# Optimization experiments

Hardware: AMD Instinct MI355X
Metric: run time of the kernel (lower is better)

The kernel has to match this reference:

```python
import jax, jax.numpy as jnp
import numpy as np

NUM_HEADS = 12

def setup_inputs() -> dict:
    key = jax.random.key(0)
    k1, k2 = jax.random.split(key)
    X = jax.random.normal(k1, (2, 2048, 768), dtype=jnp.float32)
    # torch nn.Linear(dim, 2*dim, bias=False) weight has shape [2*dim, dim]
    W_qkv = jax.random.normal(k2, (1536, 768), dtype=jnp.float32) * (768 ** -0.5)
    return {"X": X, "W_qkv": W_qkv}

def reference(X, W_qkv):
    B, N, C = X.shape
    H = NUM_HEADS
    hd = C // H
    scale = hd ** -0.5
    # qkv: [B, N, 2, H, hd]
    qkv = (X @ W_qkv.T).reshape(B, N, 2, H, hd)
    q = jnp.transpose(qkv[:, :, 0], (0, 2, 1, 3))  # [B, H, N, hd]
    k = jnp.transpose(qkv[:, :, 1], (0, 2, 1, 3))  # [B, H, N, hd]
    attn = jnp.einsum('bhnd,bhmd->bhnm', q, k) * scale  # [B, H, N, N]
    # dropout p=0 -> identity; double sum over heads and keys
    scores = attn.sum(axis=1).sum(axis=-1)  # [B, N]
    return scores
```

## Files before the change

kernel.cpp:

```cpp
#include <hip/hip_runtime.h>


#define DIM 768
#define SEQ 2048
#define NGRP 8
#define NBLK 512
#define PBASE 0xAAAAAAAAu


__global__ __launch_bounds__(256, 2)
void fused_k(const float* __restrict__ X, const float* __restrict__ W,
             float* __restrict__ out, float* __restrict__ ws) {
    float* xpart = ws;
    float* t     = ws + 2 * NGRP * DIM;
    unsigned* cw   = (unsigned*)(ws + 16384);
    unsigned* root = cw + 512;
    unsigned* cnt2 = cw + 544;

    __shared__ alignas(16) float sbuf[DIM];
    __shared__ float vloc[24];

    const int bi   = blockIdx.x;
    const int tid  = threadIdx.x;
    const int lane = tid & 63;
    const int wv   = tid >> 6;

    {
        int b  = bi >> 8;
        int ch = bi & 255;
        int g  = ch >> 5;
        if (tid < 192) {
            const float4* base =
                (const float4*)(X + ((size_t)b * SEQ + (size_t)ch * 8) * DIM) + tid;
            float4 a = {0.f, 0.f, 0.f, 0.f};
            #pragma unroll
            for (int n = 0; n < 8; ++n) {
                float4 x = base[n * 192];
                a.x += x.x; a.y += x.y; a.z += x.z; a.w += x.w;
            }
            float* dst = xpart + (size_t)(b * NGRP + g) * DIM + tid * 4;
            atomicAdd(dst + 0, a.x);
            atomicAdd(dst + 1, a.y);
            atomicAdd(dst + 2, a.z);
            atomicAdd(dst + 3, a.w);
        }
    }
    __syncthreads();
    if (tid == 0) {
        unsigned* leaf = cw + (bi & 15) * 32;
        unsigned old = __hip_atomic_fetch_add(leaf, 1u, __ATOMIC_RELAXED,
                                              __HIP_MEMORY_SCOPE_AGENT);
        if (old == PBASE + 31)
            __hip_atomic_fetch_add(root, 1u, __ATOMIC_RELAXED,
                                   __HIP_MEMORY_SCOPE_AGENT);
    }

    if (bi < 64) {
        if (tid == 0) {
            int guard = 0;
            while (__hip_atomic_load(root, __ATOMIC_RELAXED,
                                     __HIP_MEMORY_SCOPE_AGENT) != PBASE + 16) {
                __builtin_amdgcn_s_sleep(1);
                if (++guard > (1 << 24)) break;
            }
        }
        __syncthreads();

        int b     = bi >> 5;
        int chunk = bi & 31;
        int c0    = chunk * 24;

        #pragma unroll
        for (int k = 0; k < 3; ++k) {
            int d = tid + k * 256;
            const float* p = xpart + (size_t)(b * NGRP) * DIM + d;
            float s = 0.f;
            #pragma unroll
            for (int g = 0; g < NGRP; ++g)
                s += p[(size_t)g * DIM];
            sbuf[d] = s;
        }
        __syncthreads();

        const float4* xs4 = (const float4*)sbuf;
        #pragma unroll
        for (int ic = 0; ic < 6; ++ic) {
            int c = c0 + wv * 6 + ic;
            const float4* wr = (const float4*)(W + (size_t)(DIM + c) * DIM);
            float acc = 0.f;
            #pragma unroll
            for (int j = 0; j < 3; ++j) {
                float4 a = wr[lane + 64 * j];
                float4 s = xs4[lane + 64 * j];
                acc += a.x * s.x + a.y * s.y + a.z * s.z + a.w * s.w;
            }
            #pragma unroll
            for (int off = 32; off; off >>= 1) acc += __shfl_down(acc, off, 64);
            if (lane == 0) vloc[wv * 6 + ic] = acc;
        }
        __syncthreads();

        #pragma unroll
        for (int k = 0; k < 3; ++k) {
            int d = tid + k * 256;
            float acc = 0.f;
            #pragma unroll
            for (int i = 0; i < 24; ++i)
                acc += W[(size_t)(c0 + i) * DIM + d] * vloc[i];
            atomicAdd(&t[b * DIM + d], acc);
        }
        __syncthreads();
        if (tid == 0)
            __hip_atomic_fetch_add(cnt2, 1u, __ATOMIC_RELAXED,
                                   __HIP_MEMORY_SCOPE_AGENT);
    }

    if (tid == 0) {
        int guard = 0;
        while (__hip_atomic_load(cnt2, __ATOMIC_RELAXED,
                                 __HIP_MEMORY_SCOPE_AGENT) != PBASE + 64) {
            __builtin_amdgcn_s_sleep(4);
            if (++guard > (1 << 24)) break;
        }
    }
    __syncthreads();

    {
        int b = bi >> 8;
        if (tid < 192)
            ((float4*)sbuf)[tid] = ((const float4*)(t + b * DIM))[tid];
        __syncthreads();

        const float4* t4 = (const float4*)sbuf;
        int r0 = bi * 8 + wv * 2;
        #pragma unroll
        for (int rr = 0; rr < 2; ++rr) {
            int r = r0 + rr;
            const float4* xr = (const float4*)(X + (size_t)r * DIM);
            float acc = 0.f;
            #pragma unroll
            for (int j = 0; j < 3; ++j) {
                float4 a = xr[lane + 64 * j];
                float4 s = t4[lane + 64 * j];
                acc += a.x * s.x + a.y * s.y + a.z * s.z + a.w * s.w;
            }
            #pragma unroll
            for (int off = 32; off; off >>= 1) acc += __shfl_down(acc, off, 64);
            if (lane == 0) out[r] = acc * 0.125f;
        }
    }
}

extern "C" void kernel_launch(void* const* d_in, const int* in_sizes, int n_in,
                              void* d_out, int out_size, void* d_ws, size_t ws_size,
                              hipStream_t stream) {
    const float* X = (const float*)d_in[0];
    const float* W = (const float*)d_in[1];
    float* out = (float*)d_out;
    float* ws  = (float*)d_ws;

    fused_k<<<NBLK, 256, 0, stream>>>(X, W, out, ws);
}
```

Before: 84.14 us.

## Keep X tile in registers for final dot, widen phase-B across more blocks

Each block now holds its 8 rows of X in registers from the first column-sum pass and reuses them for the final score dot product, so X is not reloaded from global memory. The W-projection phase is spread over 128 blocks with 12 columns each instead of 64 blocks with 24. Those blocks also prefetch their W rows into cache before spinning on the grid barrier. The trade-off is more registers per thread (32 extra floats) and twice as many atomics into t, with a larger counter wait.

```diff
diff --git a/kernel.cpp b/kernel.cpp
--- a/kernel.cpp
+++ b/kernel.cpp
@@ -5,6 +5,7 @@
 #define SEQ 2048
 #define NGRP 8
 #define NBLK 512
+#define NB_B 128
 #define PBASE 0xAAAAAAAAu
 
 
@@ -18,13 +19,15 @@
     unsigned* cnt2 = cw + 544;
 
     __shared__ alignas(16) float sbuf[DIM];
-    __shared__ float vloc[24];
+    __shared__ float vloc[12];
+    __shared__ float red[3][8];
 
     const int bi   = blockIdx.x;
     const int tid  = threadIdx.x;
     const int lane = tid & 63;
     const int wv   = tid >> 6;
 
+    float4 xa[8];
     {
         int b  = bi >> 8;
         int ch = bi & 255;
@@ -35,8 +38,8 @@
             float4 a = {0.f, 0.f, 0.f, 0.f};
             #pragma unroll
             for (int n = 0; n < 8; ++n) {
-                float4 x = base[n * 192];
-                a.x += x.x; a.y += x.y; a.z += x.z; a.w += x.w;
+                xa[n] = base[n * 192];
+                a.x += xa[n].x; a.y += xa[n].y; a.z += xa[n].z; a.w += xa[n].w;
             }
             float* dst = xpart + (size_t)(b * NGRP + g) * DIM + tid * 4;
             atomicAdd(dst + 0, a.x);
@@ -55,7 +58,24 @@
                                    __HIP_MEMORY_SCOPE_AGENT);
     }
 
-    if (bi < 64) {
+    if (bi < NB_B) {
+        int b     = bi >> 6;
+        int chunk = bi & 63;
+        int c0    = chunk * 12;
+
+        {
+            const float4* wq4 = (const float4*)(W + (size_t)c0 * DIM);
+            const float4* wk4 = (const float4*)(W + (size_t)(DIM + c0) * DIM);
+            float dummy = 0.f;
+            #pragma unroll
+            for (int i = 0; i < 9; ++i) {
+                float4 a = wq4[tid + i * 256];
+                float4 c = wk4[tid + i * 256];
+                dummy += a.x + a.w + c.x + c.w;
+            }
+            asm volatile("" :: "v"(dummy));
+        }
+
         if (tid == 0) {
             int guard = 0;
             while (__hip_atomic_load(root, __ATOMIC_RELAXED,
@@ -65,10 +85,6 @@
             }
         }
         __syncthreads();
-
-        int b     = bi >> 5;
-        int chunk = bi & 31;
-        int c0    = chunk * 24;
 
         #pragma unroll
         for (int k = 0; k < 3; ++k) {
@@ -84,8 +100,8 @@
 
         const float4* xs4 = (const float4*)sbuf;
         #pragma unroll
-        for (int ic = 0; ic < 6; ++ic) {
-            int c = c0 + wv * 6 + ic;
+        for (int ic = 0; ic < 3; ++ic) {
+            int c = c0 + wv * 3 + ic;
             const float4* wr = (const float4*)(W + (size_t)(DIM + c) * DIM);
             float acc = 0.f;
             #pragma unroll
@@ -96,7 +112,7 @@
             }
             #pragma unroll
             for (int off = 32; off; off >>= 1) acc += __shfl_down(acc, off, 64);
-            if (lane == 0) vloc[wv * 6 + ic] = acc;
+            if (lane == 0) vloc[wv * 3 + ic] = acc;
         }
         __syncthreads();
 
@@ -105,7 +121,7 @@
             int d = tid + k * 256;
             float acc = 0.f;
             #pragma unroll
-            for (int i = 0; i < 24; ++i)
+            for (int i = 0; i < 12; ++i)
                 acc += W[(size_t)(c0 + i) * DIM + d] * vloc[i];
             atomicAdd(&t[b * DIM + d], acc);
         }
@@ -118,7 +134,7 @@
     if (tid == 0) {
         int guard = 0;
         while (__hip_atomic_load(cnt2, __ATOMIC_RELAXED,
-                                 __HIP_MEMORY_SCOPE_AGENT) != PBASE + 64) {
+                                 __HIP_MEMORY_SCOPE_AGENT) != PBASE + NB_B) {
             __builtin_amdgcn_s_sleep(4);
             if (++guard > (1 << 24)) break;
         }
@@ -131,23 +147,29 @@
             ((float4*)sbuf)[tid] = ((const float4*)(t + b * DIM))[tid];
         __syncthreads();
 
-        const float4* t4 = (const float4*)sbuf;
-        int r0 = bi * 8 + wv * 2;
-        #pragma unroll
-        for (int rr = 0; rr < 2; ++rr) {
-            int r = r0 + rr;
-            const float4* xr = (const float4*)(X + (size_t)r * DIM);
-            float acc = 0.f;
+        if (tid < 192) {
+            float4 tv = ((const float4*)sbuf)[tid];
+            float p[8];
             #pragma unroll
-            for (int j = 0; j < 3; ++j) {
-                float4 a = xr[lane + 64 * j];
-                float4 s = t4[lane + 64 * j];
-                acc += a.x * s.x + a.y * s.y + a.z * s.z + a.w * s.w;
+            for (int n = 0; n < 8; ++n)
+                p[n] = xa[n].x * tv.x + xa[n].y * tv.y
+                     + xa[n].z * tv.z + xa[n].w * tv.w;
+            #pragma unroll
+            for (int off = 32; off; off >>= 1) {
+                #pragma unroll
+                for (int n = 0; n < 8; ++n)
+                    p[n] += __shfl_down(p[n], off, 64);
             }
-            #pragma unroll
-            for (int off = 32; off; off >>= 1) acc += __shfl_down(acc, off, 64);
-            if (lane == 0) out[r] = acc * 0.125f;
+            if (lane == 0) {
+                #pragma unroll
+                for (int n = 0; n < 8; ++n)
+                    red[wv][n] = p[n];
+            }
         }
+        __syncthreads();
+        if (tid < 8)
+            out[bi * 8 + tid] =
+                0.125f * (red[0][tid] + red[1][tid] + red[2][tid]);
     }
 }
 
```

After: 84.82 us. No clear change (+0.8%).

## Shrink grid to 128 blocks with flat barriers and W prefetch during wait

Applied to the files above, without the earlier changes.

Cuts the grid from 512 to 128 blocks so every block takes part in both the W-projection phase and the final row dot products. The two-level atomic counter tree becomes a single flat counter, and each block warms its W rows into cache with dummy loads before spinning on the barrier. Each block now sums 32 rows of X and computes 32 outputs, keeping the t vector in registers. Fewer blocks means less parallelism for streaming X, but it also means fewer participants to wait for at each grid barrier.

```diff
diff --git a/kernel.cpp b/kernel.cpp
--- a/kernel.cpp
+++ b/kernel.cpp
@@ -4,72 +4,79 @@
 #define DIM 768
 #define SEQ 2048
 #define NGRP 8
-#define NBLK 512
+#define NBLK 128
 #define PBASE 0xAAAAAAAAu
 
 
-__global__ __launch_bounds__(256, 2)
+__global__ __launch_bounds__(256)
 void fused_k(const float* __restrict__ X, const float* __restrict__ W,
              float* __restrict__ out, float* __restrict__ ws) {
     float* xpart = ws;
     float* t     = ws + 2 * NGRP * DIM;
-    unsigned* cw   = (unsigned*)(ws + 16384);
-    unsigned* root = cw + 512;
-    unsigned* cnt2 = cw + 544;
+    unsigned* cnt1 = (unsigned*)(ws + 16384);
+    unsigned* cnt2 = cnt1 + 64;
 
     __shared__ alignas(16) float sbuf[DIM];
-    __shared__ float vloc[24];
+    __shared__ float vloc[12];
 
     const int bi   = blockIdx.x;
     const int tid  = threadIdx.x;
     const int lane = tid & 63;
     const int wv   = tid >> 6;
 
+    const int b  = bi >> 6;
+    const int ch = bi & 63;
+    const int c0 = ch * 12;
+
+    if (tid < 192) {
+        const float4* base =
+            (const float4*)(X + ((size_t)b * SEQ + (size_t)ch * 32) * DIM) + tid;
+        float4 a0 = {0.f, 0.f, 0.f, 0.f};
+        float4 a1 = {0.f, 0.f, 0.f, 0.f};
+        #pragma unroll
+        for (int n = 0; n < 32; n += 2) {
+            float4 x = base[n * 192];
+            float4 y = base[(n + 1) * 192];
+            a0.x += x.x; a0.y += x.y; a0.z += x.z; a0.w += x.w;
+            a1.x += y.x; a1.y += y.y; a1.z += y.z; a1.w += y.w;
+        }
+        a0.x += a1.x; a0.y += a1.y; a0.z += a1.z; a0.w += a1.w;
+        int g = ch >> 3;
+        float* dst = xpart + (size_t)(b * NGRP + g) * DIM + tid * 4;
+        atomicAdd(dst + 0, a0.x);
+        atomicAdd(dst + 1, a0.y);
+        atomicAdd(dst + 2, a0.z);
+        atomicAdd(dst + 3, a0.w);
+    }
+    __syncthreads();
+    if (tid == 0)
+        __hip_atomic_fetch_add(cnt1, 1u, __ATOMIC_RELAXED,
+                               __HIP_MEMORY_SCOPE_AGENT);
+
     {
-        int b  = bi >> 8;
-        int ch = bi & 255;
-        int g  = ch >> 5;
-        if (tid < 192) {
-            const float4* base =
-                (const float4*)(X + ((size_t)b * SEQ + (size_t)ch * 8) * DIM) + tid;
-            float4 a = {0.f, 0.f, 0.f, 0.f};
-            #pragma unroll
-            for (int n = 0; n < 8; ++n) {
-                float4 x = base[n * 192];
-                a.x += x.x; a.y += x.y; a.z += x.z; a.w += x.w;
-            }
-            float* dst = xpart + (size_t)(b * NGRP + g) * DIM + tid * 4;
-            atomicAdd(dst + 0, a.x);
-            atomicAdd(dst + 1, a.y);
-            atomicAdd(dst + 2, a.z);
-            atomicAdd(dst + 3, a.w);
+        const float4* wq4 = (const float4*)(W + (size_t)c0 * DIM);
+        const float4* wk4 = (const float4*)(W + (size_t)(DIM + c0) * DIM);
+        float dummy = 0.f;
+        #pragma unroll
+        for (int i = 0; i < 9; ++i) {
+            float4 a = wq4[tid + i * 256];
+            float4 c = wk4[tid + i * 256];
+            dummy += a.x + a.w + c.x + c.w;
+        }
+        asm volatile("" :: "v"(dummy));
+    }
+
+    if (tid == 0) {
+        int guard = 0;
+        while (__hip_atomic_load(cnt1, __ATOMIC_RELAXED,
+                                 __HIP_MEMORY_SCOPE_AGENT) != PBASE + NBLK) {
+            __builtin_amdgcn_s_sleep(1);
+            if (++guard > (1 << 24)) break;
         }
     }
     __syncthreads();
-    if (tid == 0) {
-        unsigned* leaf = cw + (bi & 15) * 32;
-        unsigned old = __hip_atomic_fetch_add(leaf, 1u, __ATOMIC_RELAXED,
-                                              __HIP_MEMORY_SCOPE_AGENT);
-        if (old == PBASE + 31)
-            __hip_atomic_fetch_add(root, 1u, __ATOMIC_RELAXED,
-                                   __HIP_MEMORY_SCOPE_AGENT);
-    }
 
-    if (bi < 64) {
-        if (tid == 0) {
-            int guard = 0;
-            while (__hip_atomic_load(root, __ATOMIC_RELAXED,
-                                     __HIP_MEMORY_SCOPE_AGENT) != PBASE + 16) {
-                __builtin_amdgcn_s_sleep(1);
-                if (++guard > (1 << 24)) break;
-            }
-        }
-        __syncthreads();
-
-        int b     = bi >> 5;
-        int chunk = bi & 31;
-        int c0    = chunk * 24;
-
+    {
         #pragma unroll
         for (int k = 0; k < 3; ++k) {
             int d = tid + k * 256;
@@ -84,8 +91,8 @@
 
         const float4* xs4 = (const float4*)sbuf;
         #pragma unroll
-        for (int ic = 0; ic < 6; ++ic) {
-            int c = c0 + wv * 6 + ic;
+        for (int ic = 0; ic < 3; ++ic) {
+            int c = c0 + wv * 3 + ic;
             const float4* wr = (const float4*)(W + (size_t)(DIM + c) * DIM);
             float acc = 0.f;
             #pragma unroll
@@ -96,7 +103,7 @@
             }
             #pragma unroll
             for (int off = 32; off; off >>= 1) acc += __shfl_down(acc, off, 64);
-            if (lane == 0) vloc[wv * 6 + ic] = acc;
+            if (lane == 0) vloc[wv * 3 + ic] = acc;
         }
         __syncthreads();
 
@@ -105,45 +112,46 @@
             int d = tid + k * 256;
             float acc = 0.f;
             #pragma unroll
-            for (int i = 0; i < 24; ++i)
+            for (int i = 0; i < 12; ++i)
                 acc += W[(size_t)(c0 + i) * DIM + d] * vloc[i];
             atomicAdd(&t[b * DIM + d], acc);
         }
-        __syncthreads();
-        if (tid == 0)
-            __hip_atomic_fetch_add(cnt2, 1u, __ATOMIC_RELAXED,
-                                   __HIP_MEMORY_SCOPE_AGENT);
     }
+    __syncthreads();
+    if (tid == 0)
+        __hip_atomic_fetch_add(cnt2, 1u, __ATOMIC_RELAXED,
+                               __HIP_MEMORY_SCOPE_AGENT);
 
     if (tid == 0) {
         int guard = 0;
         while (__hip_atomic_load(cnt2, __ATOMIC_RELAXED,
-                                 __HIP_MEMORY_SCOPE_AGENT) != PBASE + 64) {
-            __builtin_amdgcn_s_sleep(4);
+                                 __HIP_MEMORY_SCOPE_AGENT) != PBASE + NBLK) {
+            __builtin_amdgcn_s_sleep(1);
             if (++guard > (1 << 24)) break;
         }
     }
     __syncthreads();
 
     {
-        int b = bi >> 8;
         if (tid < 192)
             ((float4*)sbuf)[tid] = ((const float4*)(t + b * DIM))[tid];
         __syncthreads();
 
         const float4* t4 = (const float4*)sbuf;
-        int r0 = bi * 8 + wv * 2;
+        float4 tv0 = t4[lane];
+        float4 tv1 = t4[lane + 64];
+        float4 tv2 = t4[lane + 128];
+        int r0 = bi * 32 + wv * 8;
         #pragma unroll
-        for (int rr = 0; rr < 2; ++rr) {
+        for (int rr = 0; rr < 8; ++rr) {
             int r = r0 + rr;
             const float4* xr = (const float4*)(X + (size_t)r * DIM);
-            float acc = 0.f;
-            #pragma unroll
-            for (int j = 0; j < 3; ++j) {
-                float4 a = xr[lane + 64 * j];
-                float4 s = t4[lane + 64 * j];
-                acc += a.x * s.x + a.y * s.y + a.z * s.z + a.w * s.w;
-            }
+            float4 a = xr[lane];
+            float4 bq = xr[lane + 64];
+            float4 c = xr[lane + 128];
+            float acc = a.x * tv0.x + a.y * tv0.y + a.z * tv0.z + a.w * tv0.w
+                      + bq.x * tv1.x + bq.y * tv1.y + bq.z * tv1.z + bq.w * tv1.w
+                      + c.x * tv2.x + c.y * tv2.y + c.z * tv2.z + c.w * tv2.w;
             #pragma unroll
             for (int off = 32; off; off >>= 1) acc += __shfl_down(acc, off, 64);
             if (lane == 0) out[r] = acc * 0.125f;
```

After: 75.49 us. -10.3%, faster.
